# Kernel optimization log

Hardware: AMD Instinct MI355X
Metric: run time of the kernel (lower is better)

## Reference

```python
import jax, jax.numpy as jnp
import numpy as np
from jax import lax

B, T, I, H, O = 256, 512, 64, 128, 2  # batch, seq_len, input_size, hidden_size, output_size


def gru_layer(x, Wih, Whh, bih, bhh, reverse):
    # x: [B,T,in_dim], Wih: [3H,in_dim], Whh: [3H,H]; PyTorch gate order: r, z, n
    xw = jnp.einsum('bti,gi->btg', x, Wih) + bih  # precompute input projections [B,T,3H]

    def step(h, xw_t):
        gh = h @ Whh.T + bhh  # [B,3H]
        r = jax.nn.sigmoid(xw_t[:, :H] + gh[:, :H])
        z = jax.nn.sigmoid(xw_t[:, H:2 * H] + gh[:, H:2 * H])
        n = jnp.tanh(xw_t[:, 2 * H:] + r * gh[:, 2 * H:])
        h_new = (1.0 - z) * n + z * h
        return h_new, h_new

    h0 = jnp.zeros((x.shape[0], H), x.dtype)
    _, hs = lax.scan(step, h0, jnp.swapaxes(xw, 0, 1), reverse=reverse)
    # lax.scan with reverse=True stacks outputs aligned to original time order,
    # matching PyTorch's bidirectional GRU output layout.
    return jnp.swapaxes(hs, 0, 1)  # [B,T,H]


def gru_forward(x, params, fc_w, fc_b):
    h = x
    for (Wf, Uf, bf, cf, Wb, Ub, bb, cb) in params:
        fwd = gru_layer(h, Wf, Uf, bf, cf, reverse=False)
        bwd = gru_layer(h, Wb, Ub, bb, cb, reverse=True)
        h = jnp.concatenate([fwd, bwd], axis=-1)  # [B,T,2H]
    last = jax.nn.relu(h[:, -1, :])  # relu then take last timestep (equivalent order)
    return last @ fc_w.T + fc_b  # [B,O]


def setup_inputs() -> dict:
    key = jax.random.key(0)
    ks = iter(jax.random.split(key, 24))
    s = 1.0 / np.sqrt(H)  # PyTorch GRU init scale
    u = lambda shape: jax.random.uniform(next(ks), shape, jnp.float32, -s, s)
    inp = {"x": jax.random.normal(next(ks), (B, T, I), jnp.float32)}
    for l, in_dim in enumerate([I, 2 * H]):
        for d in ("f", "b"):
            inp[f"Wih{l}{d}"] = u((3 * H, in_dim))
            inp[f"Whh{l}{d}"] = u((3 * H, H))
            inp[f"bih{l}{d}"] = u((3 * H,))
            inp[f"bhh{l}{d}"] = u((3 * H,))
    inp["fc_w"] = u((O, 2 * H))
    inp["fc_b"] = u((O,))
    return inp


def reference(x, Wih0f, Whh0f, bih0f, bhh0f, Wih0b, Whh0b, bih0b, bhh0b,
              Wih1f, Whh1f, bih1f, bhh1f, Wih1b, Whh1b, bih1b, bhh1b,
              fc_w, fc_b):
    params = [(Wih0f, Whh0f, bih0f, bhh0f, Wih0b, Whh0b, bih0b, bhh0b),
              (Wih1f, Whh1f, bih1f, bhh1f, Wih1b, Whh1b, bih1b, bhh1b)]
    return gru_forward(x, params, fc_w, fc_b)
```

## Files before the change

### kernel.cpp

```cpp
#include <hip/hip_runtime.h>
#include <hip/hip_fp16.h>

#define B_  256
#define T_  512
#define I_  64
#define H_  128
#define G_  384
#define HC  256

#define O_OUT0 0ull
#define O_XW1  67108864ull
#define O_X16  O_XW1
#define O_WP   167772160ull
#define O_H1F  (O_WP + 196608ull)
#define O_WF16 (O_H1F + 131072ull)

typedef _Float16 h8 __attribute__((ext_vector_type(8)));
typedef _Float16 h2 __attribute__((ext_vector_type(2)));
typedef float    f4 __attribute__((ext_vector_type(4)));

__device__ __forceinline__ float sigm(float x)   { return __builtin_amdgcn_rcpf(1.f + __expf(-x)); }
__device__ __forceinline__ float tanh_f(float x) { return 1.f - 2.f * __builtin_amdgcn_rcpf(1.f + __expf(2.f * x)); }

__device__ __forceinline__ void bar_lds() {
    asm volatile("s_waitcnt lgkmcnt(0)\n\ts_barrier" ::: "memory");
}

__device__ __forceinline__ h8 load_w8(const float* src) {
    f4 a = *(const f4*)src;
    f4 b = *(const f4*)(src + 4);
    h8 v;
    v[0]=(_Float16)a[0]; v[1]=(_Float16)a[1]; v[2]=(_Float16)a[2]; v[3]=(_Float16)a[3];
    v[4]=(_Float16)b[0]; v[5]=(_Float16)b[1]; v[6]=(_Float16)b[2]; v[7]=(_Float16)b[3];
    return v;
}

__global__ void prep(const float* __restrict__ x, _Float16* __restrict__ x16,
                     const float* __restrict__ Wf, _Float16* __restrict__ wf16,
                     const float* __restrict__ W1b, __half2* __restrict__ wp) {
    const int bid = blockIdx.x;
    const int tid = threadIdx.x;
    if (bid < 4096) {
        int i = bid * 256 + tid;
        const float* s = x + (size_t)i * 8;
        f4 a = *(const f4*)s, b = *(const f4*)(s + 4);
        h8 v;
        v[0]=(_Float16)a[0]; v[1]=(_Float16)a[1]; v[2]=(_Float16)a[2]; v[3]=(_Float16)a[3];
        v[4]=(_Float16)b[0]; v[5]=(_Float16)b[1]; v[6]=(_Float16)b[2]; v[7]=(_Float16)b[3];
        *(h8*)(x16 + (size_t)i * 8) = v;
    } else if (bid < 4144) {
        int i = (bid - 4096) * 256 + tid;
        const float* s = Wf + (size_t)i * 8;
        f4 a = *(const f4*)s, b = *(const f4*)(s + 4);
        h8 v;
        v[0]=(_Float16)a[0]; v[1]=(_Float16)a[1]; v[2]=(_Float16)a[2]; v[3]=(_Float16)a[3];
        v[4]=(_Float16)b[0]; v[5]=(_Float16)b[1]; v[6]=(_Float16)b[2]; v[7]=(_Float16)b[3];
        *(h8*)(wf16 + (size_t)i * 8) = v;
    } else {
        int i = (bid - 4144) * 256 + tid;
        int c = i % G_;
        int k2 = i / G_;
        wp[i] = __halves2half2(__float2half(W1b[c * 256 + 2 * k2]),
                               __float2half(W1b[c * 256 + 2 * k2 + 1]));
    }
}

__launch_bounds__(512, 1)
__global__ void scan_l0(const _Float16* __restrict__ x16,
                        const float* __restrict__ Wih_f, const float* __restrict__ Whh_f,
                        const float* __restrict__ bih_f, const float* __restrict__ bhh_f,
                        const float* __restrict__ Wih_b, const float* __restrict__ Whh_b,
                        const float* __restrict__ bih_b, const float* __restrict__ bhh_b,
                        _Float16* __restrict__ out0) {
    __shared__ __align__(16) _Float16 s_h[2][16 * 128];

    const int tid  = threadIdx.x;
    const int lane = tid & 63;
    const int w    = tid >> 6;
    const int dir  = blockIdx.y;
    const int b0   = blockIdx.x * 4;

    const float* Wih = dir ? Wih_b : Wih_f;
    const float* Whh = dir ? Whh_b : Whh_f;
    const float* bih = dir ? bih_b : bih_f;
    const float* bhh = dir ? bhh_b : bhh_f;

    for (int i = tid; i < 2 * 16 * 128; i += 512) ((_Float16*)s_h)[i] = (_Float16)0.f;

    const int ln15 = lane & 15;
    const int lq   = lane >> 4;
    const int col  = 16 * w + ln15;

    h8 bh[3][4], bx[3][2];
    float seedR = bih[col] + bhh[col];
    float seedZ = bih[H_ + col] + bhh[H_ + col];
    float bihN  = bih[2 * H_ + col];
    float bhhN  = bhh[2 * H_ + col];
#pragma unroll
    for (int g = 0; g < 3; g++) {
        int n = g * H_ + col;
#pragma unroll
        for (int kt = 0; kt < 4; kt++) bh[g][kt] = load_w8(Whh + (size_t)n * H_ + kt * 32 + lq * 8);
#pragma unroll
        for (int kt = 0; kt < 2; kt++) bx[g][kt] = load_w8(Wih + (size_t)n * I_ + kt * 32 + lq * 8);
    }
    int offh[4];
#pragma unroll
    for (int kt = 0; kt < 4; kt++) offh[kt] = ln15 * 128 + (((kt * 4 + lq) ^ ln15) & 15) * 8;
    const int row0  = lq * 4;
    const int offw0 = row0 * 128 + ((((col >> 3) ^ row0) & 15)) * 8 + (col & 7);

    const _Float16* xbase = x16 + ((size_t)(b0 + (ln15 >> 2)) * T_) * I_ + lq * 8;
    _Float16* obase = out0 + ((size_t)(b0 + lq) * T_) * HC + dir * H_ + col;

    __syncthreads();

    float hF = 0.f;
    h8 xA[2], xB[2];
    {
        int t0 = dir ? (T_ - 1) : 0;
        int t1 = dir ? (T_ - 2) : 1;
        xA[0] = *(const h8*)(xbase + (size_t)t0 * I_);
        xA[1] = *(const h8*)(xbase + (size_t)t0 * I_ + 32);
        xB[0] = *(const h8*)(xbase + (size_t)t1 * I_);
        xB[1] = *(const h8*)(xbase + (size_t)t1 * I_ + 32);
    }

#pragma unroll 1
    for (int s = 0; s < T_; s += 2) {
        {
            h8 ah0 = *(const h8*)&s_h[0][offh[0]];
            h8 ah1 = *(const h8*)&s_h[0][offh[1]];
            h8 ah2 = *(const h8*)&s_h[0][offh[2]];
            h8 ah3 = *(const h8*)&s_h[0][offh[3]];
            f4 aR  = (f4){seedR, seedR, seedR, seedR};
            f4 aZ  = (f4){seedZ, seedZ, seedZ, seedZ};
            f4 aXn = (f4){bihN, bihN, bihN, bihN};
            f4 aHn = (f4){bhhN, bhhN, bhhN, bhhN};
            aR  = __builtin_amdgcn_mfma_f32_16x16x32_f16(xA[0], bx[0][0], aR, 0, 0, 0);
            aZ  = __builtin_amdgcn_mfma_f32_16x16x32_f16(xA[0], bx[1][0], aZ, 0, 0, 0);
            aXn = __builtin_amdgcn_mfma_f32_16x16x32_f16(xA[0], bx[2][0], aXn, 0, 0, 0);
            aR  = __builtin_amdgcn_mfma_f32_16x16x32_f16(xA[1], bx[0][1], aR, 0, 0, 0);
            aZ  = __builtin_amdgcn_mfma_f32_16x16x32_f16(xA[1], bx[1][1], aZ, 0, 0, 0);
            aXn = __builtin_amdgcn_mfma_f32_16x16x32_f16(xA[1], bx[2][1], aXn, 0, 0, 0);
            aR  = __builtin_amdgcn_mfma_f32_16x16x32_f16(ah0, bh[0][0], aR, 0, 0, 0);
            aZ  = __builtin_amdgcn_mfma_f32_16x16x32_f16(ah0, bh[1][0], aZ, 0, 0, 0);
            aHn = __builtin_amdgcn_mfma_f32_16x16x32_f16(ah0, bh[2][0], aHn, 0, 0, 0);
            aR  = __builtin_amdgcn_mfma_f32_16x16x32_f16(ah1, bh[0][1], aR, 0, 0, 0);
            aZ  = __builtin_amdgcn_mfma_f32_16x16x32_f16(ah1, bh[1][1], aZ, 0, 0, 0);
            aHn = __builtin_amdgcn_mfma_f32_16x16x32_f16(ah1, bh[2][1], aHn, 0, 0, 0);
            aR  = __builtin_amdgcn_mfma_f32_16x16x32_f16(ah2, bh[0][2], aR, 0, 0, 0);
            aZ  = __builtin_amdgcn_mfma_f32_16x16x32_f16(ah2, bh[1][2], aZ, 0, 0, 0);
            aHn = __builtin_amdgcn_mfma_f32_16x16x32_f16(ah2, bh[2][2], aHn, 0, 0, 0);
            aR  = __builtin_amdgcn_mfma_f32_16x16x32_f16(ah3, bh[0][3], aR, 0, 0, 0);
            aZ  = __builtin_amdgcn_mfma_f32_16x16x32_f16(ah3, bh[1][3], aZ, 0, 0, 0);
            aHn = __builtin_amdgcn_mfma_f32_16x16x32_f16(ah3, bh[2][3], aHn, 0, 0, 0);
            if (s + 2 < T_) {
                int tn = dir ? (T_ - 3 - s) : (s + 2);
                xA[0] = *(const h8*)(xbase + (size_t)tn * I_);
                xA[1] = *(const h8*)(xbase + (size_t)tn * I_ + 32);
            }
            float r = sigm(aR[0]);
            float z = sigm(aZ[0]);
            float n = tanh_f(aXn[0] + r * aHn[0]);
            float h = n + z * (hF - n);
            hF = h;
            s_h[1][offw0] = (_Float16)h;
            int ta = dir ? (T_ - 1 - s) : s;
            obase[(size_t)ta * HC] = (_Float16)h;
            bar_lds();
        }
        {
            h8 ah0 = *(const h8*)&s_h[1][offh[0]];
            h8 ah1 = *(const h8*)&s_h[1][offh[1]];
            h8 ah2 = *(const h8*)&s_h[1][offh[2]];
            h8 ah3 = *(const h8*)&s_h[1][offh[3]];
            f4 aR  = (f4){seedR, seedR, seedR, seedR};
            f4 aZ  = (f4){seedZ, seedZ, seedZ, seedZ};
            f4 aXn = (f4){bihN, bihN, bihN, bihN};
            f4 aHn = (f4){bhhN, bhhN, bhhN, bhhN};
            aR  = __builtin_amdgcn_mfma_f32_16x16x32_f16(xB[0], bx[0][0], aR, 0, 0, 0);
            aZ  = __builtin_amdgcn_mfma_f32_16x16x32_f16(xB[0], bx[1][0], aZ, 0, 0, 0);
            aXn = __builtin_amdgcn_mfma_f32_16x16x32_f16(xB[0], bx[2][0], aXn, 0, 0, 0);
            aR  = __builtin_amdgcn_mfma_f32_16x16x32_f16(xB[1], bx[0][1], aR, 0, 0, 0);
            aZ  = __builtin_amdgcn_mfma_f32_16x16x32_f16(xB[1], bx[1][1], aZ, 0, 0, 0);
            aXn = __builtin_amdgcn_mfma_f32_16x16x32_f16(xB[1], bx[2][1], aXn, 0, 0, 0);
            aR  = __builtin_amdgcn_mfma_f32_16x16x32_f16(ah0, bh[0][0], aR, 0, 0, 0);
            aZ  = __builtin_amdgcn_mfma_f32_16x16x32_f16(ah0, bh[1][0], aZ, 0, 0, 0);
            aHn = __builtin_amdgcn_mfma_f32_16x16x32_f16(ah0, bh[2][0], aHn, 0, 0, 0);
            aR  = __builtin_amdgcn_mfma_f32_16x16x32_f16(ah1, bh[0][1], aR, 0, 0, 0);
            aZ  = __builtin_amdgcn_mfma_f32_16x16x32_f16(ah1, bh[1][1], aZ, 0, 0, 0);
            aHn = __builtin_amdgcn_mfma_f32_16x16x32_f16(ah1, bh[2][1], aHn, 0, 0, 0);
            aR  = __builtin_amdgcn_mfma_f32_16x16x32_f16(ah2, bh[0][2], aR, 0, 0, 0);
            aZ  = __builtin_amdgcn_mfma_f32_16x16x32_f16(ah2, bh[1][2], aZ, 0, 0, 0);
            aHn = __builtin_amdgcn_mfma_f32_16x16x32_f16(ah2, bh[2][2], aHn, 0, 0, 0);
            aR  = __builtin_amdgcn_mfma_f32_16x16x32_f16(ah3, bh[0][3], aR, 0, 0, 0);
            aZ  = __builtin_amdgcn_mfma_f32_16x16x32_f16(ah3, bh[1][3], aZ, 0, 0, 0);
            aHn = __builtin_amdgcn_mfma_f32_16x16x32_f16(ah3, bh[2][3], aHn, 0, 0, 0);
            if (s + 3 < T_) {
                int tn = dir ? (T_ - 4 - s) : (s + 3);
                xB[0] = *(const h8*)(xbase + (size_t)tn * I_);
                xB[1] = *(const h8*)(xbase + (size_t)tn * I_ + 32);
            }
            float r = sigm(aR[0]);
            float z = sigm(aZ[0]);
            float n = tanh_f(aXn[0] + r * aHn[0]);
            float h = n + z * (hF - n);
            hF = h;
            s_h[0][offw0] = (_Float16)h;
            int ta = dir ? (T_ - 2 - s) : (s + 1);
            obase[(size_t)ta * HC] = (_Float16)h;
            bar_lds();
        }
    }
}

__launch_bounds__(256, 1)
__global__ void gemm_xw1(const _Float16* __restrict__ A,
                         const _Float16* __restrict__ Bw,
                         const float* __restrict__ bias,
                         _Float16* __restrict__ C) {
    __shared__ __align__(16) _Float16 sA[2][64 * 64];
    __shared__ __align__(16) _Float16 sB[2][384 * 64];
    const int tid  = threadIdx.x;
    const int lane = tid & 63;
    const int w    = tid >> 6;
    const int wm   = w & 1, wn = w >> 1;
    const int ln15 = lane & 15, lq = lane >> 4;
    const size_t m0 = (size_t)blockIdx.x * 64;

    f4 acc[2][12] = {};

    int aRow[2], aG[2], aOff[2];
#pragma unroll
    for (int k = 0; k < 2; k++) {
        int idx = k * 256 + tid;
        aRow[k] = idx >> 3; aG[k] = idx & 7;
        aOff[k] = aRow[k] * 64 + ((aG[k] ^ (aRow[k] & 7)) & 7) * 8;
    }
    int bRow[12], bG[12], bOff[12];
#pragma unroll
    for (int k = 0; k < 12; k++) {
        int idx = k * 256 + tid;
        bRow[k] = idx >> 3; bG[k] = idx & 7;
        bOff[k] = bRow[k] * 64 + ((bG[k] ^ (bRow[k] & 7)) & 7) * 8;
    }
    int offA[2][2], offB[12][2];
#pragma unroll
    for (int mt = 0; mt < 2; mt++)
#pragma unroll
        for (int kt = 0; kt < 2; kt++) {
            int row = wm * 32 + mt * 16 + ln15;
            offA[mt][kt] = row * 64 + (((kt * 4 + lq) ^ (row & 7)) & 7) * 8;
        }
#pragma unroll
    for (int nt = 0; nt < 12; nt++)
#pragma unroll
        for (int kt = 0; kt < 2; kt++) {
            int row = wn * 192 + nt * 16 + ln15;
            offB[nt][kt] = row * 64 + (((kt * 4 + lq) ^ (row & 7)) & 7) * 8;
        }

    {
        h8 av[2], bv[12];
#pragma unroll
        for (int k = 0; k < 2; k++) av[k] = *(const h8*)(A + (m0 + aRow[k]) * 256 + aG[k] * 8);
#pragma unroll
        for (int k = 0; k < 12; k++) bv[k] = *(const h8*)(Bw + (size_t)bRow[k] * 256 + bG[k] * 8);
#pragma unroll
        for (int k = 0; k < 2; k++) *(h8*)&sA[0][aOff[k]] = av[k];
#pragma unroll
        for (int k = 0; k < 12; k++) *(h8*)&sB[0][bOff[k]] = bv[k];
        bar_lds();
    }

#pragma unroll
    for (int c = 0; c < 4; c++) {
        const int cur = c & 1;
        h8 av[2], bv[12];
        if (c < 3) {
#pragma unroll
            for (int k = 0; k < 2; k++)
                av[k] = *(const h8*)(A + (m0 + aRow[k]) * 256 + (c + 1) * 64 + aG[k] * 8);
#pragma unroll
            for (int k = 0; k < 12; k++)
                bv[k] = *(const h8*)(Bw + (size_t)bRow[k] * 256 + (c + 1) * 64 + bG[k] * 8);
        }
#pragma unroll
        for (int kt = 0; kt < 2; kt++) {
            h8 af0 = *(const h8*)&sA[cur][offA[0][kt]];
            h8 af1 = *(const h8*)&sA[cur][offA[1][kt]];
#pragma unroll
            for (int nt = 0; nt < 12; nt++) {
                h8 bf = *(const h8*)&sB[cur][offB[nt][kt]];
                acc[0][nt] = __builtin_amdgcn_mfma_f32_16x16x32_f16(af0, bf, acc[0][nt], 0, 0, 0);
                acc[1][nt] = __builtin_amdgcn_mfma_f32_16x16x32_f16(af1, bf, acc[1][nt], 0, 0, 0);
            }
        }
        if (c < 3) {
#pragma unroll
            for (int k = 0; k < 2; k++) *(h8*)&sA[cur ^ 1][aOff[k]] = av[k];
#pragma unroll
            for (int k = 0; k < 12; k++) *(h8*)&sB[cur ^ 1][bOff[k]] = bv[k];
            bar_lds();
        }
    }
#pragma unroll
    for (int nt = 0; nt < 12; nt++) {
        int col = wn * 192 + nt * 16 + ln15;
        float bb = bias[col];
        int pcol = (col < 256) ? ((col & 127) * 2 + (col >> 7)) : col;
#pragma unroll
        for (int mt = 0; mt < 2; mt++) {
            size_t row = m0 + wm * 32 + mt * 16 + lq * 4;
#pragma unroll
            for (int reg = 0; reg < 4; reg++)
                C[(row + reg) * G_ + pcol] = (_Float16)(acc[mt][nt][reg] + bb);
        }
    }
}

__launch_bounds__(512, 1)
__global__ void scan_l1(const _Float16* __restrict__ xw1,
                        const float* __restrict__ Whh,
                        const float* __restrict__ bhh,
                        float* __restrict__ h1f) {
    __shared__ __align__(16) _Float16 s_h[2][16 * 128];

    const int tid  = threadIdx.x;
    const int lane = tid & 63;
    const int w    = tid >> 6;
    const int b0   = blockIdx.x * 4;

    for (int i = tid; i < 2 * 16 * 128; i += 512) ((_Float16*)s_h)[i] = (_Float16)0.f;

    const int ln15 = lane & 15;
    const int lq   = lane >> 4;
    const int col  = 16 * w + ln15;

    h8 bh[3][4];
    float bhhF[3];
#pragma unroll
    for (int g = 0; g < 3; g++) {
        int n = g * H_ + col;
        bhhF[g] = bhh[n];
#pragma unroll
        for (int kt = 0; kt < 4; kt++) bh[g][kt] = load_w8(Whh + (size_t)n * H_ + kt * 32 + lq * 8);
    }
    int offh[4];
#pragma unroll
    for (int kt = 0; kt < 4; kt++) offh[kt] = ln15 * 128 + (((kt * 4 + lq) ^ ln15) & 15) * 8;
    const int row0  = lq * 4;
    const int offw0 = row0 * 128 + ((((col >> 3) ^ row0) & 15)) * 8 + (col & 7);

    const _Float16* rzbase = xw1 + ((size_t)(b0 + lq) * T_) * G_ + 2 * col;
    const _Float16* nbase  = xw1 + ((size_t)(b0 + lq) * T_) * G_ + 256 + col;

    __syncthreads();

    float hF = 0.f;
    h2 rzA = *(const h2*)(rzbase);
    h2 rzB = *(const h2*)(rzbase + G_);
    _Float16 nA = *nbase;
    _Float16 nB = *(nbase + G_);

#pragma unroll 1
    for (int s = 0; s < T_; s += 2) {
        {
            h8 ah0 = *(const h8*)&s_h[0][offh[0]];
            h8 ah1 = *(const h8*)&s_h[0][offh[1]];
            h8 ah2 = *(const h8*)&s_h[0][offh[2]];
            h8 ah3 = *(const h8*)&s_h[0][offh[3]];
            float xr = (float)rzA[0], xz = (float)rzA[1], xn = (float)nA;
            if (s + 2 < T_) {
                rzA = *(const h2*)(rzbase + (size_t)(s + 2) * G_);
                nA  = *(nbase + (size_t)(s + 2) * G_);
            }
            f4 aR  = (f4){bhhF[0], bhhF[0], bhhF[0], bhhF[0]};
            f4 aZ  = (f4){bhhF[1], bhhF[1], bhhF[1], bhhF[1]};
            f4 aHn = (f4){bhhF[2], bhhF[2], bhhF[2], bhhF[2]};
            aR  = __builtin_amdgcn_mfma_f32_16x16x32_f16(ah0, bh[0][0], aR, 0, 0, 0);
            aZ  = __builtin_amdgcn_mfma_f32_16x16x32_f16(ah0, bh[1][0], aZ, 0, 0, 0);
            aHn = __builtin_amdgcn_mfma_f32_16x16x32_f16(ah0, bh[2][0], aHn, 0, 0, 0);
            aR  = __builtin_amdgcn_mfma_f32_16x16x32_f16(ah1, bh[0][1], aR, 0, 0, 0);
            aZ  = __builtin_amdgcn_mfma_f32_16x16x32_f16(ah1, bh[1][1], aZ, 0, 0, 0);
            aHn = __builtin_amdgcn_mfma_f32_16x16x32_f16(ah1, bh[2][1], aHn, 0, 0, 0);
            aR  = __builtin_amdgcn_mfma_f32_16x16x32_f16(ah2, bh[0][2], aR, 0, 0, 0);
            aZ  = __builtin_amdgcn_mfma_f32_16x16x32_f16(ah2, bh[1][2], aZ, 0, 0, 0);
            aHn = __builtin_amdgcn_mfma_f32_16x16x32_f16(ah2, bh[2][2], aHn, 0, 0, 0);
            aR  = __builtin_amdgcn_mfma_f32_16x16x32_f16(ah3, bh[0][3], aR, 0, 0, 0);
            aZ  = __builtin_amdgcn_mfma_f32_16x16x32_f16(ah3, bh[1][3], aZ, 0, 0, 0);
            aHn = __builtin_amdgcn_mfma_f32_16x16x32_f16(ah3, bh[2][3], aHn, 0, 0, 0);
            float r = sigm(xr + aR[0]);
            float z = sigm(xz + aZ[0]);
            float n = tanh_f(xn + r * aHn[0]);
            float h = n + z * (hF - n);
            hF = h;
            s_h[1][offw0] = (_Float16)h;
            bar_lds();
        }
        {
            h8 ah0 = *(const h8*)&s_h[1][offh[0]];
            h8 ah1 = *(const h8*)&s_h[1][offh[1]];
            h8 ah2 = *(const h8*)&s_h[1][offh[2]];
            h8 ah3 = *(const h8*)&s_h[1][offh[3]];
            float xr = (float)rzB[0], xz = (float)rzB[1], xn = (float)nB;
            if (s + 3 < T_) {
                rzB = *(const h2*)(rzbase + (size_t)(s + 3) * G_);
                nB  = *(nbase + (size_t)(s + 3) * G_);
            }
            f4 aR  = (f4){bhhF[0], bhhF[0], bhhF[0], bhhF[0]};
            f4 aZ  = (f4){bhhF[1], bhhF[1], bhhF[1], bhhF[1]};
            f4 aHn = (f4){bhhF[2], bhhF[2], bhhF[2], bhhF[2]};
            aR  = __builtin_amdgcn_mfma_f32_16x16x32_f16(ah0, bh[0][0], aR, 0, 0, 0);
            aZ  = __builtin_amdgcn_mfma_f32_16x16x32_f16(ah0, bh[1][0], aZ, 0, 0, 0);
            aHn = __builtin_amdgcn_mfma_f32_16x16x32_f16(ah0, bh[2][0], aHn, 0, 0, 0);
            aR  = __builtin_amdgcn_mfma_f32_16x16x32_f16(ah1, bh[0][1], aR, 0, 0, 0);
            aZ  = __builtin_amdgcn_mfma_f32_16x16x32_f16(ah1, bh[1][1], aZ, 0, 0, 0);
            aHn = __builtin_amdgcn_mfma_f32_16x16x32_f16(ah1, bh[2][1], aHn, 0, 0, 0);
            aR  = __builtin_amdgcn_mfma_f32_16x16x32_f16(ah2, bh[0][2], aR, 0, 0, 0);
            aZ  = __builtin_amdgcn_mfma_f32_16x16x32_f16(ah2, bh[1][2], aZ, 0, 0, 0);
            aHn = __builtin_amdgcn_mfma_f32_16x16x32_f16(ah2, bh[2][2], aHn, 0, 0, 0);
            aR  = __builtin_amdgcn_mfma_f32_16x16x32_f16(ah3, bh[0][3], aR, 0, 0, 0);
            aZ  = __builtin_amdgcn_mfma_f32_16x16x32_f16(ah3, bh[1][3], aZ, 0, 0, 0);
            aHn = __builtin_amdgcn_mfma_f32_16x16x32_f16(ah3, bh[2][3], aHn, 0, 0, 0);
            float r = sigm(xr + aR[0]);
            float z = sigm(xz + aZ[0]);
            float n = tanh_f(xn + r * aHn[0]);
            float h = n + z * (hF - n);
            hF = h;
            s_h[0][offw0] = (_Float16)h;
            bar_lds();
        }
    }
    h1f[(size_t)(b0 + lq) * H_ + col] = hF;
}

__launch_bounds__(384)
__global__ void final_k(const _Float16* __restrict__ out0,
                        const float* __restrict__ h1f,
                        const __half2* __restrict__ w1b,
                        const float* __restrict__ bih1b, const float* __restrict__ bhh1b,
                        const float* __restrict__ fcw, const float* __restrict__ fcb,
                        float* __restrict__ out) {
    __shared__ __align__(16) float s_x1[HC];
    __shared__ __align__(16) float s_xw[G_];
    __shared__ __align__(16) float s_hc[HC];
    __shared__ float s_red[8];
    const int tid = threadIdx.x;
    const int b = blockIdx.x;
    if (tid < HC)
        s_x1[tid] = (float)out0[((size_t)b * T_ + (T_ - 1)) * HC + tid];
    __syncthreads();
    {
        float acc0 = 0.f, acc1 = 0.f;
        const float2* xv = (const float2*)s_x1;
#pragma unroll 8
        for (int k2 = 0; k2 < 128; k2 += 2) {
            float2 w0 = __half22float2(w1b[k2 * G_ + tid]);
            float2 w1 = __half22float2(w1b[(k2 + 1) * G_ + tid]);
            float2 a0 = xv[k2], a1 = xv[k2 + 1];
            acc0 += a0.x * w0.x + a0.y * w0.y;
            acc1 += a1.x * w1.x + a1.y * w1.y;
        }
        s_xw[tid] = bih1b[tid] + acc0 + acc1;
    }
    __syncthreads();
    if (tid < H_) {
        int j = tid;
        float rg = sigm(s_xw[j] + bhh1b[j]);
        float zg = sigm(s_xw[H_ + j] + bhh1b[H_ + j]);
        float ng = tanh_f(s_xw[2 * H_ + j] + rg * bhh1b[2 * H_ + j]);
        float hb = (1.f - zg) * ng;
        s_hc[H_ + j] = fmaxf(hb, 0.f);
        s_hc[j] = fmaxf(h1f[(size_t)b * H_ + j], 0.f);
    }
    __syncthreads();
    if (tid < HC) {
        float hv = s_hc[tid];
        float p0 = hv * fcw[tid];
        float p1 = hv * fcw[HC + tid];
#pragma unroll
        for (int off = 32; off; off >>= 1) {
            p0 += __shfl_down(p0, off);
            p1 += __shfl_down(p1, off);
        }
        if ((tid & 63) == 0) { s_red[(tid >> 6) * 2] = p0; s_red[(tid >> 6) * 2 + 1] = p1; }
    }
    __syncthreads();
    if (tid == 0) {
        out[b * 2 + 0] = fcb[0] + s_red[0] + s_red[2] + s_red[4] + s_red[6];
        out[b * 2 + 1] = fcb[1] + s_red[1] + s_red[3] + s_red[5] + s_red[7];
    }
}

extern "C" void kernel_launch(void* const* d_in, const int* in_sizes, int n_in,
                              void* d_out, int out_size, void* d_ws, size_t ws_size,
                              hipStream_t stream) {
    (void)in_sizes; (void)n_in; (void)out_size; (void)ws_size;
    const float* x     = (const float*)d_in[0];
    const float* Wih0f = (const float*)d_in[1];
    const float* Whh0f = (const float*)d_in[2];
    const float* bih0f = (const float*)d_in[3];
    const float* bhh0f = (const float*)d_in[4];
    const float* Wih0b = (const float*)d_in[5];
    const float* Whh0b = (const float*)d_in[6];
    const float* bih0b = (const float*)d_in[7];
    const float* bhh0b = (const float*)d_in[8];
    const float* Wih1f = (const float*)d_in[9];
    const float* Whh1f = (const float*)d_in[10];
    const float* bih1f = (const float*)d_in[11];
    const float* bhh1f = (const float*)d_in[12];
    const float* Wih1b = (const float*)d_in[13];
    const float* bih1b = (const float*)d_in[15];
    const float* bhh1b = (const float*)d_in[16];
    const float* fcw   = (const float*)d_in[17];
    const float* fcb   = (const float*)d_in[18];

    char* ws = (char*)d_ws;
    _Float16* out0 = (_Float16*)(ws + O_OUT0);
    _Float16* xw1  = (_Float16*)(ws + O_XW1);
    _Float16* x16  = (_Float16*)(ws + O_X16);
    __half2*  wp   = (__half2*)(ws + O_WP);
    float*    h1f  = (float*)(ws + O_H1F);
    _Float16* wf16 = (_Float16*)(ws + O_WF16);
    float*    out  = (float*)d_out;

    prep<<<4336, 256, 0, stream>>>(x, x16, Wih1f, wf16, Wih1b, wp);

    scan_l0<<<dim3(64, 2), 512, 0, stream>>>(x16, Wih0f, Whh0f, bih0f, bhh0f,
                                             Wih0b, Whh0b, bih0b, bhh0b, out0);

    gemm_xw1<<<2048, 256, 0, stream>>>(out0, wf16, bih1f, xw1);

    scan_l1<<<64, 512, 0, stream>>>(xw1, Whh1f, bhh1f, h1f);

    final_k<<<256, 384, 0, stream>>>(out0, h1f, wp, bih1b, bhh1b, fcw, fcb, out);
}
```

Measured before the change: 678.9 us.

## Move input-projection MFMAs off the recurrence critical path and split accumulation chains

The layer-0 kernel now computes the input projection for the next timestep after the hidden-state update and before the barrier, so those MFMAs overlap the synchronisation wait instead of lengthening each step's dependency chain. In both recurrent kernels the hidden-state MFMA accumulation is split into two independent chains (k-tiles 0/1 and 2/3) that are summed at the end, halving the dependent MFMA chain depth. Lanes whose A-fragment rows are unused now read a fixed LDS location, which reduces bank traffic. The changes add registers for prefetched x vectors and precomputed projections, and alter the summation order slightly.

```diff
diff --git a/kernel.cpp b/kernel.cpp
--- a/kernel.cpp
+++ b/kernel.cpp
@@ -104,70 +104,90 @@
 #pragma unroll
         for (int kt = 0; kt < 2; kt++) bx[g][kt] = load_w8(Wih + (size_t)n * I_ + kt * 32 + lq * 8);
     }
+    const bool avalid = (ln15 & 3) == 0;
     int offh[4];
 #pragma unroll
-    for (int kt = 0; kt < 4; kt++) offh[kt] = ln15 * 128 + (((kt * 4 + lq) ^ ln15) & 15) * 8;
+    for (int kt = 0; kt < 4; kt++)
+        offh[kt] = avalid ? (ln15 * 128 + (((kt * 4 + lq) ^ ln15) & 15) * 8) : 128;
     const int row0  = lq * 4;
     const int offw0 = row0 * 128 + ((((col >> 3) ^ row0) & 15)) * 8 + (col & 7);
 
     const _Float16* xbase = x16 + ((size_t)(b0 + (ln15 >> 2)) * T_) * I_ + lq * 8;
     _Float16* obase = out0 + ((size_t)(b0 + lq) * T_) * HC + dir * H_ + col;
 
-    __syncthreads();
+    const f4 z4 = (f4){0.f, 0.f, 0.f, 0.f};
+    const f4 sR4 = (f4){seedR, seedR, seedR, seedR};
+    const f4 sZ4 = (f4){seedZ, seedZ, seedZ, seedZ};
+    const f4 sXn4 = (f4){bihN, bihN, bihN, bihN};
+    const f4 sHn4 = (f4){bhhN, bhhN, bhhN, bhhN};
 
     float hF = 0.f;
-    h8 xA[2], xB[2];
+    float xr0, xz0, xn0, xr1, xz1, xn1;
+    h8 xvA0, xvA1, xvB0, xvB1;
     {
         int t0 = dir ? (T_ - 1) : 0;
         int t1 = dir ? (T_ - 2) : 1;
-        xA[0] = *(const h8*)(xbase + (size_t)t0 * I_);
-        xA[1] = *(const h8*)(xbase + (size_t)t0 * I_ + 32);
-        xB[0] = *(const h8*)(xbase + (size_t)t1 * I_);
-        xB[1] = *(const h8*)(xbase + (size_t)t1 * I_ + 32);
-    }
+        int t2 = dir ? (T_ - 3) : 2;
+        h8 xc0 = *(const h8*)(xbase + (size_t)t0 * I_);
+        h8 xc1 = *(const h8*)(xbase + (size_t)t0 * I_ + 32);
+        xvA0 = *(const h8*)(xbase + (size_t)t1 * I_);
+        xvA1 = *(const h8*)(xbase + (size_t)t1 * I_ + 32);
+        xvB0 = *(const h8*)(xbase + (size_t)t2 * I_);
+        xvB1 = *(const h8*)(xbase + (size_t)t2 * I_ + 32);
+        f4 aXr = sR4, aXz = sZ4, aXn = sXn4;
+        aXr = __builtin_amdgcn_mfma_f32_16x16x32_f16(xc0, bx[0][0], aXr, 0, 0, 0);
+        aXr = __builtin_amdgcn_mfma_f32_16x16x32_f16(xc1, bx[0][1], aXr, 0, 0, 0);
+        aXz = __builtin_amdgcn_mfma_f32_16x16x32_f16(xc0, bx[1][0], aXz, 0, 0, 0);
+        aXz = __builtin_amdgcn_mfma_f32_16x16x32_f16(xc1, bx[1][1], aXz, 0, 0, 0);
+        aXn = __builtin_amdgcn_mfma_f32_16x16x32_f16(xc0, bx[2][0], aXn, 0, 0, 0);
+        aXn = __builtin_amdgcn_mfma_f32_16x16x32_f16(xc1, bx[2][1], aXn, 0, 0, 0);
+        xr0 = aXr[0]; xz0 = aXz[0]; xn0 = aXn[0];
+    }
+    __syncthreads();
 
 #pragma unroll 1
-    for (int s = 0; s < T_; s += 2) {
+    for (int t = 0; t < T_; t += 2) {
         {
             h8 ah0 = *(const h8*)&s_h[0][offh[0]];
             h8 ah1 = *(const h8*)&s_h[0][offh[1]];
             h8 ah2 = *(const h8*)&s_h[0][offh[2]];
             h8 ah3 = *(const h8*)&s_h[0][offh[3]];
-            f4 aR  = (f4){seedR, seedR, seedR, seedR};
-            f4 aZ  = (f4){seedZ, seedZ, seedZ, seedZ};
-            f4 aXn = (f4){bihN, bihN, bihN, bihN};
-            f4 aHn = (f4){bhhN, bhhN, bhhN, bhhN};
-            aR  = __builtin_amdgcn_mfma_f32_16x16x32_f16(xA[0], bx[0][0], aR, 0, 0, 0);
-            aZ  = __builtin_amdgcn_mfma_f32_16x16x32_f16(xA[0], bx[1][0], aZ, 0, 0, 0);
-            aXn = __builtin_amdgcn_mfma_f32_16x16x32_f16(xA[0], bx[2][0], aXn, 0, 0, 0);
-            aR  = __builtin_amdgcn_mfma_f32_16x16x32_f16(xA[1], bx[0][1], aR, 0, 0, 0);
-            aZ  = __builtin_amdgcn_mfma_f32_16x16x32_f16(xA[1], bx[1][1], aZ, 0, 0, 0);
-            aXn = __builtin_amdgcn_mfma_f32_16x16x32_f16(xA[1], bx[2][1], aXn, 0, 0, 0);
-            aR  = __builtin_amdgcn_mfma_f32_16x16x32_f16(ah0, bh[0][0], aR, 0, 0, 0);
-            aZ  = __builtin_amdgcn_mfma_f32_16x16x32_f16(ah0, bh[1][0], aZ, 0, 0, 0);
-            aHn = __builtin_amdgcn_mfma_f32_16x16x32_f16(ah0, bh[2][0], aHn, 0, 0, 0);
-            aR  = __builtin_amdgcn_mfma_f32_16x16x32_f16(ah1, bh[0][1], aR, 0, 0, 0);
-            aZ  = __builtin_amdgcn_mfma_f32_16x16x32_f16(ah1, bh[1][1], aZ, 0, 0, 0);
-            aHn = __builtin_amdgcn_mfma_f32_16x16x32_f16(ah1, bh[2][1], aHn, 0, 0, 0);
-            aR  = __builtin_amdgcn_mfma_f32_16x16x32_f16(ah2, bh[0][2], aR, 0, 0, 0);
-            aZ  = __builtin_amdgcn_mfma_f32_16x16x32_f16(ah2, bh[1][2], aZ, 0, 0, 0);
-            aHn = __builtin_amdgcn_mfma_f32_16x16x32_f16(ah2, bh[2][2], aHn, 0, 0, 0);
-            aR  = __builtin_amdgcn_mfma_f32_16x16x32_f16(ah3, bh[0][3], aR, 0, 0, 0);
-            aZ  = __builtin_amdgcn_mfma_f32_16x16x32_f16(ah3, bh[1][3], aZ, 0, 0, 0);
-            aHn = __builtin_amdgcn_mfma_f32_16x16x32_f16(ah3, bh[2][3], aHn, 0, 0, 0);
-            if (s + 2 < T_) {
-                int tn = dir ? (T_ - 3 - s) : (s + 2);
-                xA[0] = *(const h8*)(xbase + (size_t)tn * I_);
-                xA[1] = *(const h8*)(xbase + (size_t)tn * I_ + 32);
-            }
-            float r = sigm(aR[0]);
-            float z = sigm(aZ[0]);
-            float n = tanh_f(aXn[0] + r * aHn[0]);
+            f4 hRa = z4, hRb = z4, hZa = z4, hZb = z4, hNa = sHn4, hNb = z4;
+            hRa = __builtin_amdgcn_mfma_f32_16x16x32_f16(ah0, bh[0][0], hRa, 0, 0, 0);
+            hZa = __builtin_amdgcn_mfma_f32_16x16x32_f16(ah0, bh[1][0], hZa, 0, 0, 0);
+            hNa = __builtin_amdgcn_mfma_f32_16x16x32_f16(ah0, bh[2][0], hNa, 0, 0, 0);
+            hRb = __builtin_amdgcn_mfma_f32_16x16x32_f16(ah2, bh[0][2], hRb, 0, 0, 0);
+            hZb = __builtin_amdgcn_mfma_f32_16x16x32_f16(ah2, bh[1][2], hZb, 0, 0, 0);
+            hNb = __builtin_amdgcn_mfma_f32_16x16x32_f16(ah2, bh[2][2], hNb, 0, 0, 0);
+            hRa = __builtin_amdgcn_mfma_f32_16x16x32_f16(ah1, bh[0][1], hRa, 0, 0, 0);
+            hZa = __builtin_amdgcn_mfma_f32_16x16x32_f16(ah1, bh[1][1], hZa, 0, 0, 0);
+            hNa = __builtin_amdgcn_mfma_f32_16x16x32_f16(ah1, bh[2][1], hNa, 0, 0, 0);
+            hRb = __builtin_amdgcn_mfma_f32_16x16x32_f16(ah3, bh[0][3], hRb, 0, 0, 0);
+            hZb = __builtin_amdgcn_mfma_f32_16x16x32_f16(ah3, bh[1][3], hZb, 0, 0, 0);
+            hNb = __builtin_amdgcn_mfma_f32_16x16x32_f16(ah3, bh[2][3], hNb, 0, 0, 0);
+            float r = sigm(xr0 + hRa[0] + hRb[0]);
+            float z = sigm(xz0 + hZa[0] + hZb[0]);
+            float n = tanh_f(xn0 + r * (hNa[0] + hNb[0]));
             float h = n + z * (hF - n);
             hF = h;
             s_h[1][offw0] = (_Float16)h;
-            int ta = dir ? (T_ - 1 - s) : s;
+            int ta = dir ? (T_ - 1 - t) : t;
             obase[(size_t)ta * HC] = (_Float16)h;
+            {
+                f4 aXr = sR4, aXz = sZ4, aXn = sXn4;
+                aXr = __builtin_amdgcn_mfma_f32_16x16x32_f16(xvA0, bx[0][0], aXr, 0, 0, 0);
+                aXr = __builtin_amdgcn_mfma_f32_16x16x32_f16(xvA1, bx[0][1], aXr, 0, 0, 0);
+                aXz = __builtin_amdgcn_mfma_f32_16x16x32_f16(xvA0, bx[1][0], aXz, 0, 0, 0);
+                aXz = __builtin_amdgcn_mfma_f32_16x16x32_f16(xvA1, bx[1][1], aXz, 0, 0, 0);
+                aXn = __builtin_amdgcn_mfma_f32_16x16x32_f16(xvA0, bx[2][0], aXn, 0, 0, 0);
+                aXn = __builtin_amdgcn_mfma_f32_16x16x32_f16(xvA1, bx[2][1], aXn, 0, 0, 0);
+                xr1 = aXr[0]; xz1 = aXz[0]; xn1 = aXn[0];
+            }
+            if (t + 3 < T_) {
+                int tn = dir ? (T_ - 4 - t) : (t + 3);
+                xvA0 = *(const h8*)(xbase + (size_t)tn * I_);
+                xvA1 = *(const h8*)(xbase + (size_t)tn * I_ + 32);
+            }
             bar_lds();
         }
         {
@@ -175,41 +195,42 @@
             h8 ah1 = *(const h8*)&s_h[1][offh[1]];
             h8 ah2 = *(const h8*)&s_h[1][offh[2]];
             h8 ah3 = *(const h8*)&s_h[1][offh[3]];
-            f4 aR  = (f4){seedR, seedR, seedR, seedR};
-            f4 aZ  = (f4){seedZ, seedZ, seedZ, seedZ};
-            f4 aXn = (f4){bihN, bihN, bihN, bihN};
-            f4 aHn = (f4){bhhN, bhhN, bhhN, bhhN};
-            aR  = __builtin_amdgcn_mfma_f32_16x16x32_f16(xB[0], bx[0][0], aR, 0, 0, 0);
-            aZ  = __builtin_amdgcn_mfma_f32_16x16x32_f16(xB[0], bx[1][0], aZ, 0, 0, 0);
-            aXn = __builtin_amdgcn_mfma_f32_16x16x32_f16(xB[0], bx[2][0], aXn, 0, 0, 0);
-            aR  = __builtin_amdgcn_mfma_f32_16x16x32_f16(xB[1], bx[0][1], aR, 0, 0, 0);
-            aZ  = __builtin_amdgcn_mfma_f32_16x16x32_f16(xB[1], bx[1][1], aZ, 0, 0, 0);
-            aXn = __builtin_amdgcn_mfma_f32_16x16x32_f16(xB[1], bx[2][1], aXn, 0, 0, 0);
-            aR  = __builtin_amdgcn_mfma_f32_16x16x32_f16(ah0, bh[0][0], aR, 0, 0, 0);
-            aZ  = __builtin_amdgcn_mfma_f32_16x16x32_f16(ah0, bh[1][0], aZ, 0, 0, 0);
-            aHn = __builtin_amdgcn_mfma_f32_16x16x32_f16(ah0, bh[2][0], aHn, 0, 0, 0);
-            aR  = __builtin_amdgcn_mfma_f32_16x16x32_f16(ah1, bh[0][1], aR, 0, 0, 0);
-            aZ  = __builtin_amdgcn_mfma_f32_16x16x32_f16(ah1, bh[1][1], aZ, 0, 0, 0);
-            aHn = __builtin_amdgcn_mfma_f32_16x16x32_f16(ah1, bh[2][1], aHn, 0, 0, 0);
-            aR  = __builtin_amdgcn_mfma_f32_16x16x32_f16(ah2, bh[0][2], aR, 0, 0, 0);
-            aZ  = __builtin_amdgcn_mfma_f32_16x16x32_f16(ah2, bh[1][2], aZ, 0, 0, 0);
-            aHn = __builtin_amdgcn_mfma_f32_16x16x32_f16(ah2, bh[2][2], aHn, 0, 0, 0);
-            aR  = __builtin_amdgcn_mfma_f32_16x16x32_f16(ah3, bh[0][3], aR, 0, 0, 0);
-            aZ  = __builtin_amdgcn_mfma_f32_16x16x32_f16(ah3, bh[1][3], aZ, 0, 0, 0);
-            aHn = __builtin_amdgcn_mfma_f32_16x16x32_f16(ah3, bh[2][3], aHn, 0, 0, 0);
-            if (s + 3 < T_) {
-                int tn = dir ? (T_ - 4 - s) : (s + 3);
-                xB[0] = *(const h8*)(xbase + (size_t)tn * I_);
-                xB[1] = *(const h8*)(xbase + (size_t)tn * I_ + 32);
-            }
-            float r = sigm(aR[0]);
-            float z = sigm(aZ[0]);
-            float n = tanh_f(aXn[0] + r * aHn[0]);
+            f4 hRa = z4, hRb = z4, hZa = z4, hZb = z4, hNa = sHn4, hNb = z4;
+            hRa = __builtin_amdgcn_mfma_f32_16x16x32_f16(ah0, bh[0][0], hRa, 0, 0, 0);
+            hZa = __builtin_amdgcn_mfma_f32_16x16x32_f16(ah0, bh[1][0], hZa, 0, 0, 0);
+            hNa = __builtin_amdgcn_mfma_f32_16x16x32_f16(ah0, bh[2][0], hNa, 0, 0, 0);
+            hRb = __builtin_amdgcn_mfma_f32_16x16x32_f16(ah2, bh[0][2], hRb, 0, 0, 0);
+            hZb = __builtin_amdgcn_mfma_f32_16x16x32_f16(ah2, bh[1][2], hZb, 0, 0, 0);
+            hNb = __builtin_amdgcn_mfma_f32_16x16x32_f16(ah2, bh[2][2], hNb, 0, 0, 0);
+            hRa = __builtin_amdgcn_mfma_f32_16x16x32_f16(ah1, bh[0][1], hRa, 0, 0, 0);
+            hZa = __builtin_amdgcn_mfma_f32_16x16x32_f16(ah1, bh[1][1], hZa, 0, 0, 0);
+            hNa = __builtin_amdgcn_mfma_f32_16x16x32_f16(ah1, bh[2][1], hNa, 0, 0, 0);
+            hRb = __builtin_amdgcn_mfma_f32_16x16x32_f16(ah3, bh[0][3], hRb, 0, 0, 0);
+            hZb = __builtin_amdgcn_mfma_f32_16x16x32_f16(ah3, bh[1][3], hZb, 0, 0, 0);
+            hNb = __builtin_amdgcn_mfma_f32_16x16x32_f16(ah3, bh[2][3], hNb, 0, 0, 0);
+            float r = sigm(xr1 + hRa[0] + hRb[0]);
+            float z = sigm(xz1 + hZa[0] + hZb[0]);
+            float n = tanh_f(xn1 + r * (hNa[0] + hNb[0]));
             float h = n + z * (hF - n);
             hF = h;
             s_h[0][offw0] = (_Float16)h;
-            int ta = dir ? (T_ - 2 - s) : (s + 1);
+            int ta = dir ? (T_ - 2 - t) : (t + 1);
             obase[(size_t)ta * HC] = (_Float16)h;
+            if (t + 2 < T_) {
+                f4 aXr = sR4, aXz = sZ4, aXn = sXn4;
+                aXr = __builtin_amdgcn_mfma_f32_16x16x32_f16(xvB0, bx[0][0], aXr, 0, 0, 0);
+                aXr = __builtin_amdgcn_mfma_f32_16x16x32_f16(xvB1, bx[0][1], aXr, 0, 0, 0);
+                aXz = __builtin_amdgcn_mfma_f32_16x16x32_f16(xvB0, bx[1][0], aXz, 0, 0, 0);
+                aXz = __builtin_amdgcn_mfma_f32_16x16x32_f16(xvB1, bx[1][1], aXz, 0, 0, 0);
+                aXn = __builtin_amdgcn_mfma_f32_16x16x32_f16(xvB0, bx[2][0], aXn, 0, 0, 0);
+                aXn = __builtin_amdgcn_mfma_f32_16x16x32_f16(xvB1, bx[2][1], aXn, 0, 0, 0);
+                xr0 = aXr[0]; xz0 = aXz[0]; xn0 = aXn[0];
+            }
+            if (t + 4 < T_) {
+                int tn = dir ? (T_ - 5 - t) : (t + 4);
+                xvB0 = *(const h8*)(xbase + (size_t)tn * I_);
+                xvB1 = *(const h8*)(xbase + (size_t)tn * I_ + 32);
+            }
             bar_lds();
         }
     }
@@ -347,14 +368,21 @@
 #pragma unroll
         for (int kt = 0; kt < 4; kt++) bh[g][kt] = load_w8(Whh + (size_t)n * H_ + kt * 32 + lq * 8);
     }
+    const bool avalid = (ln15 & 3) == 0;
     int offh[4];
 #pragma unroll
-    for (int kt = 0; kt < 4; kt++) offh[kt] = ln15 * 128 + (((kt * 4 + lq) ^ ln15) & 15) * 8;
+    for (int kt = 0; kt < 4; kt++)
+        offh[kt] = avalid ? (ln15 * 128 + (((kt * 4 + lq) ^ ln15) & 15) * 8) : 128;
     const int row0  = lq * 4;
     const int offw0 = row0 * 128 + ((((col >> 3) ^ row0) & 15)) * 8 + (col & 7);
 
     const _Float16* rzbase = xw1 + ((size_t)(b0 + lq) * T_) * G_ + 2 * col;
     const _Float16* nbase  = xw1 + ((size_t)(b0 + lq) * T_) * G_ + 256 + col;
+
+    const f4 z4 = (f4){0.f, 0.f, 0.f, 0.f};
+    const f4 sR4 = (f4){bhhF[0], bhhF[0], bhhF[0], bhhF[0]};
+    const f4 sZ4 = (f4){bhhF[1], bhhF[1], bhhF[1], bhhF[1]};
+    const f4 sN4 = (f4){bhhF[2], bhhF[2], bhhF[2], bhhF[2]};
 
     __syncthreads();
 
@@ -376,24 +404,22 @@
                 rzA = *(const h2*)(rzbase + (size_t)(s + 2) * G_);
                 nA  = *(nbase + (size_t)(s + 2) * G_);
             }
-            f4 aR  = (f4){bhhF[0], bhhF[0], bhhF[0], bhhF[0]};
-            f4 aZ  = (f4){bhhF[1], bhhF[1], bhhF[1], bhhF[1]};
-            f4 aHn = (f4){bhhF[2], bhhF[2], bhhF[2], bhhF[2]};
-            aR  = __builtin_amdgcn_mfma_f32_16x16x32_f16(ah0, bh[0][0], aR, 0, 0, 0);
-            aZ  = __builtin_amdgcn_mfma_f32_16x16x32_f16(ah0, bh[1][0], aZ, 0, 0, 0);
-            aHn = __builtin_amdgcn_mfma_f32_16x16x32_f16(ah0, bh[2][0], aHn, 0, 0, 0);
-            aR  = __builtin_amdgcn_mfma_f32_16x16x32_f16(ah1, bh[0][1], aR, 0, 0, 0);
-            aZ  = __builtin_amdgcn_mfma_f32_16x16x32_f16(ah1, bh[1][1], aZ, 0, 0, 0);
-            aHn = __builtin_amdgcn_mfma_f32_16x16x32_f16(ah1, bh[2][1], aHn, 0, 0, 0);
-            aR  = __builtin_amdgcn_mfma_f32_16x16x32_f16(ah2, bh[0][2], aR, 0, 0, 0);
-            aZ  = __builtin_amdgcn_mfma_f32_16x16x32_f16(ah2, bh[1][2], aZ, 0, 0, 0);
-            aHn = __builtin_amdgcn_mfma_f32_16x16x32_f16(ah2, bh[2][2], aHn, 0, 0, 0);
-            aR  = __builtin_amdgcn_mfma_f32_16x16x32_f16(ah3, bh[0][3], aR, 0, 0, 0);
-            aZ  = __builtin_amdgcn_mfma_f32_16x16x32_f16(ah3, bh[1][3], aZ, 0, 0, 0);
-            aHn = __builtin_amdgcn_mfma_f32_16x16x32_f16(ah3, bh[2][3], aHn, 0, 0, 0);
-            float r = sigm(xr + aR[0]);
-            float z = sigm(xz + aZ[0]);
-            float n = tanh_f(xn + r * aHn[0]);
+            f4 hRa = sR4, hRb = z4, hZa = sZ4, hZb = z4, hNa = sN4, hNb = z4;
+            hRa = __builtin_amdgcn_mfma_f32_16x16x32_f16(ah0, bh[0][0], hRa, 0, 0, 0);
+            hZa = __builtin_amdgcn_mfma_f32_16x16x32_f16(ah0, bh[1][0], hZa, 0, 0, 0);
+            hNa = __builtin_amdgcn_mfma_f32_16x16x32_f16(ah0, bh[2][0], hNa, 0, 0, 0);
+            hRb = __builtin_amdgcn_mfma_f32_16x16x32_f16(ah2, bh[0][2], hRb, 0, 0, 0);
+            hZb = __builtin_amdgcn_mfma_f32_16x16x32_f16(ah2, bh[1][2], hZb, 0, 0, 0);
+            hNb = __builtin_amdgcn_mfma_f32_16x16x32_f16(ah2, bh[2][2], hNb, 0, 0, 0);
+            hRa = __builtin_amdgcn_mfma_f32_16x16x32_f16(ah1, bh[0][1], hRa, 0, 0, 0);
+            hZa = __builtin_amdgcn_mfma_f32_16x16x32_f16(ah1, bh[1][1], hZa, 0, 0, 0);
+            hNa = __builtin_amdgcn_mfma_f32_16x16x32_f16(ah1, bh[2][1], hNa, 0, 0, 0);
+            hRb = __builtin_amdgcn_mfma_f32_16x16x32_f16(ah3, bh[0][3], hRb, 0, 0, 0);
+            hZb = __builtin_amdgcn_mfma_f32_16x16x32_f16(ah3, bh[1][3], hZb, 0, 0, 0);
+            hNb = __builtin_amdgcn_mfma_f32_16x16x32_f16(ah3, bh[2][3], hNb, 0, 0, 0);
+            float r = sigm(xr + hRa[0] + hRb[0]);
+            float z = sigm(xz + hZa[0] + hZb[0]);
+            float n = tanh_f(xn + r * (hNa[0] + hNb[0]));
             float h = n + z * (hF - n);
             hF = h;
             s_h[1][offw0] = (_Float16)h;
@@ -409,24 +435,22 @@
                 rzB = *(const h2*)(rzbase + (size_t)(s + 3) * G_);
                 nB  = *(nbase + (size_t)(s + 3) * G_);
             }
-            f4 aR  = (f4){bhhF[0], bhhF[0], bhhF[0], bhhF[0]};
-            f4 aZ  = (f4){bhhF[1], bhhF[1], bhhF[1], bhhF[1]};
-            f4 aHn = (f4){bhhF[2], bhhF[2], bhhF[2], bhhF[2]};
-            aR  = __builtin_amdgcn_mfma_f32_16x16x32_f16(ah0, bh[0][0], aR, 0, 0, 0);
-            aZ  = __builtin_amdgcn_mfma_f32_16x16x32_f16(ah0, bh[1][0], aZ, 0, 0, 0);
-            aHn = __builtin_amdgcn_mfma_f32_16x16x32_f16(ah0, bh[2][0], aHn, 0, 0, 0);
-            aR  = __builtin_amdgcn_mfma_f32_16x16x32_f16(ah1, bh[0][1], aR, 0, 0, 0);
-            aZ  = __builtin_amdgcn_mfma_f32_16x16x32_f16(ah1, bh[1][1], aZ, 0, 0, 0);
-            aHn = __builtin_amdgcn_mfma_f32_16x16x32_f16(ah1, bh[2][1], aHn, 0, 0, 0);
-            aR  = __builtin_amdgcn_mfma_f32_16x16x32_f16(ah2, bh[0][2], aR, 0, 0, 0);
-            aZ  = __builtin_amdgcn_mfma_f32_16x16x32_f16(ah2, bh[1][2], aZ, 0, 0, 0);
-            aHn = __builtin_amdgcn_mfma_f32_16x16x32_f16(ah2, bh[2][2], aHn, 0, 0, 0);
-            aR  = __builtin_amdgcn_mfma_f32_16x16x32_f16(ah3, bh[0][3], aR, 0, 0, 0);
-            aZ  = __builtin_amdgcn_mfma_f32_16x16x32_f16(ah3, bh[1][3], aZ, 0, 0, 0);
-            aHn = __builtin_amdgcn_mfma_f32_16x16x32_f16(ah3, bh[2][3], aHn, 0, 0, 0);
-            float r = sigm(xr + aR[0]);
-            float z = sigm(xz + aZ[0]);
-            float n = tanh_f(xn + r * aHn[0]);
+            f4 hRa = sR4, hRb = z4, hZa = sZ4, hZb = z4, hNa = sN4, hNb = z4;
+            hRa = __builtin_amdgcn_mfma_f32_16x16x32_f16(ah0, bh[0][0], hRa, 0, 0, 0);
+            hZa = __builtin_amdgcn_mfma_f32_16x16x32_f16(ah0, bh[1][0], hZa, 0, 0, 0);
+            hNa = __builtin_amdgcn_mfma_f32_16x16x32_f16(ah0, bh[2][0], hNa, 0, 0, 0);
+            hRb = __builtin_amdgcn_mfma_f32_16x16x32_f16(ah2, bh[0][2], hRb, 0, 0, 0);
+            hZb = __builtin_amdgcn_mfma_f32_16x16x32_f16(ah2, bh[1][2], hZb, 0, 0, 0);
+            hNb = __builtin_amdgcn_mfma_f32_16x16x32_f16(ah2, bh[2][2], hNb, 0, 0, 0);
+            hRa = __builtin_amdgcn_mfma_f32_16x16x32_f16(ah1, bh[0][1], hRa, 0, 0, 0);
+            hZa = __builtin_amdgcn_mfma_f32_16x16x32_f16(ah1, bh[1][1], hZa, 0, 0, 0);
+            hNa = __builtin_amdgcn_mfma_f32_16x16x32_f16(ah1, bh[2][1], hNa, 0, 0, 0);
+            hRb = __builtin_amdgcn_mfma_f32_16x16x32_f16(ah3, bh[0][3], hRb, 0, 0, 0);
+            hZb = __builtin_amdgcn_mfma_f32_16x16x32_f16(ah3, bh[1][3], hZb, 0, 0, 0);
+            hNb = __builtin_amdgcn_mfma_f32_16x16x32_f16(ah3, bh[2][3], hNb, 0, 0, 0);
+            float r = sigm(xr + hRa[0] + hRb[0]);
+            float z = sigm(xz + hZa[0] + hZb[0]);
+            float n = tanh_f(xn + r * (hNa[0] + hNb[0]));
             float h = n + z * (hF - n);
             hF = h;
             s_h[0][offw0] = (_Float16)h;
```

New measurement: 611.7 us. 9.9% less time.
